# Optimization experiments

Hardware: AMD Instinct MI355X
Metric: run time of the kernel (lower is better)

## Reference

```python
import jax, jax.numpy as jnp
import numpy as np
from jax import lax

B, IN, H1, H2, NC = 16384, 128, 256, 128, 10
BETA = 0.5
THR = 1.0
SLOPE = 25.0  # snntorch surrogate.fast_sigmoid default slope


@jax.custom_vjp
def spike(x):
    # Heaviside fire with fast-sigmoid surrogate gradient
    return (x > 0).astype(x.dtype)

def _spike_fwd(x):
    return spike(x), x

def _spike_bwd(x, g):
    return (g / (SLOPE * jnp.abs(x) + 1.0) ** 2,)

spike.defvjp(_spike_fwd, _spike_bwd)


def setup_inputs() -> dict:
    key = jax.random.key(0)
    ks = jax.random.split(key, 7)
    def lin(kw, kb, fan_in, fan_out):
        lim = 1.0 / np.sqrt(fan_in)
        W = jax.random.uniform(kw, (fan_out, fan_in), jnp.float32, -lim, lim)
        b = jax.random.uniform(kb, (fan_out,), jnp.float32, -lim, lim)
        return W, b
    W1, b1 = lin(ks[0], ks[1], IN, H1)
    W2, b2 = lin(ks[2], ks[3], H1, H2)
    Wo, bo = lin(ks[4], ks[5], H2, NC)
    x = jax.random.normal(ks[6], (B, IN), jnp.float32)
    return {"x": x, "W1": W1, "b1": b1, "W2": W2, "b2": b2,
            "Wo": Wo, "bo": bo, "num_steps": 20}


def reference(x, W1, b1, W2, b2, Wo, bo, num_steps):
    # fc1(x) is time-invariant -> hoist out of the recurrent loop (same math)
    cur1 = x @ W1.T + b1  # [B, H1]

    def lif(mem, cur):
        # snntorch Leaky (reset_mechanism='subtract'):
        # reset from previous mem (detached), then decay+input, then fire
        reset = lax.stop_gradient((mem > THR).astype(mem.dtype))
        mem = BETA * mem + cur - reset * THR
        spk = spike(mem - THR)
        return spk, mem

    def step(carry, _):
        m1, m2, mo = carry
        s1, m1 = lif(m1, cur1)
        s2, m2 = lif(m2, s1 @ W2.T + b2)
        so, mo = lif(mo, s2 @ Wo.T + bo)
        return (m1, m2, mo), so

    init = (jnp.zeros((B, H1), x.dtype),
            jnp.zeros((B, H2), x.dtype),
            jnp.zeros((B, NC), x.dtype))
    _, spk_rec = lax.scan(step, init, None, length=num_steps)
    return spk_rec.sum(axis=0)  # [B, NC] spike counts
```

## Files before the change

### kernel.cpp

```cpp
#include <hip/hip_runtime.h>
#include <stdint.h>

#define B_TOT 16384
#define IN_DIM 128
#define H1 256
#define H2 128
#define NC 10

#define W2T_BYTES (H1 * H2 * 4)
#define WOT_OFF   W2T_BYTES
#define WOT_BYTES (H2 * NC * 4)
#define SCR_OFF   (WOT_OFF + WOT_BYTES)
#define LDS_BYTES (SCR_OFF + 16 * 1024)

typedef float v2f __attribute__((ext_vector_type(2)));

__global__ __launch_bounds__(256) void gemm1_kernel(
    const float* __restrict__ x, const float* __restrict__ W1,
    const float* __restrict__ b1, float* __restrict__ cur1) {
  __shared__ float xs[16 * 128];
  const int tid = threadIdx.x;
  const long row0 = (long)blockIdx.x * 16;

  const float4* xt = (const float4*)(x + row0 * IN_DIM);
  float4* xs4 = (float4*)xs;
  xs4[tid] = xt[tid];
  xs4[tid + 256] = xt[tid + 256];
  __syncthreads();

  const int n = tid;
  float acc[16];
#pragma unroll
  for (int r = 0; r < 16; ++r) acc[r] = 0.f;

  const float* wrow = W1 + n * IN_DIM;
  for (int k0 = 0; k0 < IN_DIM; k0 += 4) {
    const float4 wv = *(const float4*)(wrow + k0);
#pragma unroll
    for (int r = 0; r < 16; ++r) {
      const float4 xv = *(const float4*)(xs + r * IN_DIM + k0);
      acc[r] = fmaf(wv.x, xv.x, acc[r]);
      acc[r] = fmaf(wv.y, xv.y, acc[r]);
      acc[r] = fmaf(wv.z, xv.z, acc[r]);
      acc[r] = fmaf(wv.w, xv.w, acc[r]);
    }
  }
  const float bias = b1[n];
#pragma unroll
  for (int r = 0; r < 16; ++r)
    cur1[(row0 + r) * H1 + n] = acc[r] + bias;
}

__global__ __launch_bounds__(1024) void transpose_kernel(
    const float* __restrict__ W2, const float* __restrict__ Wo,
    float* __restrict__ W2T, float* __restrict__ WoT) {
  const int idx = blockIdx.x * 1024 + threadIdx.x;
  if (idx < H2 * H1) {
    const int o = idx >> 8;
    const int j = idx & 255;
    W2T[j * H2 + o] = W2[idx];
  } else {
    const int k = idx - H2 * H1;
    if (k < NC * H2) {
      const int o = k >> 7;
      const int j = k & 127;
      WoT[j * NC + o] = Wo[k];
    }
  }
}

__device__ __forceinline__ int mbcnt64(unsigned long long m) {
  return (int)__builtin_amdgcn_mbcnt_hi(
      (unsigned)(m >> 32), __builtin_amdgcn_mbcnt_lo((unsigned)m, 0u));
}

__global__ __launch_bounds__(1024) void snn_kernel(
    const float* __restrict__ cur1,
    const float* __restrict__ W2Tg, const float* __restrict__ WoTg,
    const float* __restrict__ W2, const float* __restrict__ Wo,
    const float* __restrict__ x, const float* __restrict__ W1,
    const float* __restrict__ b1,
    const float* __restrict__ b2, const float* __restrict__ bo,
    const int* __restrict__ nsp, float* __restrict__ out) {
  extern __shared__ float lds[];
  float* w2t = lds;
  float* wot = lds + H1 * H2;

  const int tid = threadIdx.x;
  if (W2Tg != nullptr) {
    float4* dst = (float4*)w2t;
    const float4* src = (const float4*)W2Tg;
#pragma unroll
    for (int i = 0; i < 8; ++i) dst[tid + i * 1024] = src[tid + i * 1024];
    if (tid < 320) ((float4*)wot)[tid] = ((const float4*)WoTg)[tid];
  } else {
    for (int idx = tid; idx < H2 * H1; idx += 1024) {
      const int o = idx >> 8;
      const int j = idx & 255;
      w2t[j * H2 + o] = W2[idx];
    }
    for (int idx = tid; idx < NC * H2; idx += 1024) {
      const int o = idx >> 7;
      const int j = idx & 127;
      wot[j * NC + o] = Wo[idx];
    }
  }
  __syncthreads();

  const int w = tid >> 6;
  const int l = tid & 63;
  const int lo = (l < NC) ? l : 0;
  const float bb0 = b2[2 * l];
  const float bb1 = b2[2 * l + 1];
  const float bol = bo[lo];
  const int nsteps = *nsp;

  int* scr = (int*)((char*)lds + SCR_OFF) + w * 256;
  const char* w2b = (const char*)lds + 8 * l;
  const char* wob = (const char*)lds + WOT_OFF + 4 * lo;

  const int wr0 = l << 9;
  const int wr1 = (64 + l) << 9;
  const int wr2 = (128 + l) << 9;
  const int wr3 = (192 + l) << 9;
  const int or0 = 80 * l;
  const int or1 = 80 * l + 40;

#define MAIN_B8()                                     \
  {                                                   \
    const int4 ia = *(const int4*)(scr + k);          \
    const int4 ib = *(const int4*)(scr + k + 4);      \
    const v2f p0 = *(const v2f*)(w2b + ia.x);         \
    const v2f p1 = *(const v2f*)(w2b + ia.y);         \
    const v2f p2 = *(const v2f*)(w2b + ia.z);         \
    const v2f p3 = *(const v2f*)(w2b + ia.w);         \
    const v2f p4 = *(const v2f*)(w2b + ib.x);         \
    const v2f p5 = *(const v2f*)(w2b + ib.y);         \
    const v2f p6 = *(const v2f*)(w2b + ib.z);         \
    const v2f p7 = *(const v2f*)(w2b + ib.w);         \
    acc += p0; acc += p1; acc += p2; acc += p3;       \
    acc += p4; acc += p5; acc += p6; acc += p7;       \
  }

#define OUT_B8()                                      \
  {                                                   \
    const int4 ia = *(const int4*)(scr + k);          \
    const int4 ib = *(const int4*)(scr + k + 4);      \
    const float q0 = *(const float*)(wob + ia.x);     \
    const float q1 = *(const float*)(wob + ia.y);     \
    const float q2 = *(const float*)(wob + ia.z);     \
    const float q3 = *(const float*)(wob + ia.w);     \
    const float q4 = *(const float*)(wob + ib.x);     \
    const float q5 = *(const float*)(wob + ib.y);     \
    const float q6 = *(const float*)(wob + ib.z);     \
    const float q7 = *(const float*)(wob + ib.w);     \
    co += q0; co += q1; co += q2; co += q3;           \
    co += q4; co += q5; co += q6; co += q7;           \
  }

  for (int r = 0; r < 4; ++r) {
    const long b = (long)blockIdx.x * 64 + w * 4 + r;

    float c[4];
    if (cur1 != nullptr) {
#pragma unroll
      for (int i = 0; i < 4; ++i) c[i] = cur1[b * H1 + i * 64 + l];
    } else {
      const float* xr = x + b * IN_DIM;
#pragma unroll
      for (int i = 0; i < 4; ++i) {
        const int n = i * 64 + l;
        const float* wr = W1 + n * IN_DIM;
        float a = 0.f;
        for (int kk = 0; kk < IN_DIM; kk += 4) {
          const float4 wv = *(const float4*)(wr + kk);
          const float4 xv = *(const float4*)(xr + kk);
          a = fmaf(wv.x, xv.x, a);
          a = fmaf(wv.y, xv.y, a);
          a = fmaf(wv.z, xv.z, a);
          a = fmaf(wv.w, xv.w, a);
        }
        c[i] = a + b1[n];
      }
    }

    float m1[4] = {0.f, 0.f, 0.f, 0.f};
    float sp1[4] = {0.f, 0.f, 0.f, 0.f};
    float m2a = 0.f, m2b = 0.f, sp2a = 0.f, sp2b = 0.f;
    float mo = 0.f, spo = 0.f, cnt = 0.f;

    for (int t = 0; t < nsteps; ++t) {
      float n0 = fmaf(0.5f, m1[0], c[0]) - sp1[0];
      float n1 = fmaf(0.5f, m1[1], c[1]) - sp1[1];
      float n2 = fmaf(0.5f, m1[2], c[2]) - sp1[2];
      float n3 = fmaf(0.5f, m1[3], c[3]) - sp1[3];
      const bool s0 = n0 > 1.0f;
      const bool s1 = n1 > 1.0f;
      const bool s2 = n2 > 1.0f;
      const bool s3 = n3 > 1.0f;
      m1[0] = n0; m1[1] = n1; m1[2] = n2; m1[3] = n3;
      sp1[0] = s0 ? 1.0f : 0.0f;
      sp1[1] = s1 ? 1.0f : 0.0f;
      sp1[2] = s2 ? 1.0f : 0.0f;
      sp1[3] = s3 ? 1.0f : 0.0f;
      const unsigned long long g0 = __ballot(s0);
      const unsigned long long g1 = __ballot(s1);
      const unsigned long long g2 = __ballot(s2);
      const unsigned long long g3 = __ballot(s3);
      const int pc0 = (int)__popcll(g0);
      const int pc1 = (int)__popcll(g1);
      const int pc2 = (int)__popcll(g2);
      const int pc3 = (int)__popcll(g3);
      const int S = pc0 + pc1 + pc2 + pc3;

      if (s0) scr[mbcnt64(g0)] = wr0;
      if (s1) scr[pc0 + mbcnt64(g1)] = wr1;
      if (s2) scr[pc0 + pc1 + mbcnt64(g2)] = wr2;
      if (s3) scr[pc0 + pc1 + pc2 + mbcnt64(g3)] = wr3;
      asm volatile("s_waitcnt lgkmcnt(0)" ::: "memory");

      v2f acc = {0.f, 0.f};
      int k = 0;
      for (; k + 8 <= S; k += 8) MAIN_B8();
      if (S & 4) {
        const int4 ia = *(const int4*)(scr + k);
        const v2f p0 = *(const v2f*)(w2b + ia.x);
        const v2f p1 = *(const v2f*)(w2b + ia.y);
        const v2f p2 = *(const v2f*)(w2b + ia.z);
        const v2f p3 = *(const v2f*)(w2b + ia.w);
        acc += p0; acc += p1; acc += p2; acc += p3;
        k += 4;
      }
      if (S & 2) {
        const int2 ia = *(const int2*)(scr + k);
        const v2f p0 = *(const v2f*)(w2b + ia.x);
        const v2f p1 = *(const v2f*)(w2b + ia.y);
        acc += p0; acc += p1;
        k += 2;
      }
      if (S & 1) {
        const int i0 = scr[k];
        const v2f p0 = *(const v2f*)(w2b + i0);
        acc += p0;
      }
      const float a0 = acc.x + bb0;
      const float a1 = acc.y + bb1;

      m2a = fmaf(0.5f, m2a, a0) - sp2a;
      m2b = fmaf(0.5f, m2b, a1) - sp2b;
      const bool sa = m2a > 1.0f;
      const bool sb = m2b > 1.0f;
      const unsigned long long mA = __ballot(sa);
      const unsigned long long mB = __ballot(sb);
      sp2a = sa ? 1.0f : 0.0f;
      sp2b = sb ? 1.0f : 0.0f;
      const int pcA = (int)__popcll(mA);
      const int So = pcA + (int)__popcll(mB);

      if (sa) scr[mbcnt64(mA)] = or0;
      if (sb) scr[pcA + mbcnt64(mB)] = or1;
      asm volatile("s_waitcnt lgkmcnt(0)" ::: "memory");

      float co = 0.f;
      k = 0;
      for (; k + 8 <= So; k += 8) OUT_B8();
      if (So & 4) {
        const int4 ia = *(const int4*)(scr + k);
        const float q0 = *(const float*)(wob + ia.x);
        const float q1 = *(const float*)(wob + ia.y);
        const float q2 = *(const float*)(wob + ia.z);
        const float q3 = *(const float*)(wob + ia.w);
        co += q0; co += q1; co += q2; co += q3;
        k += 4;
      }
      if (So & 2) {
        const int2 ia = *(const int2*)(scr + k);
        const float q0 = *(const float*)(wob + ia.x);
        const float q1 = *(const float*)(wob + ia.y);
        co += q0; co += q1;
        k += 2;
      }
      if (So & 1) {
        const int i0 = scr[k];
        co += *(const float*)(wob + i0);
      }
      co += bol;

      mo = fmaf(0.5f, mo, co) - spo;
      const bool so = mo > 1.0f;
      spo = so ? 1.0f : 0.0f;
      cnt += spo;
    }

    if (l < NC) out[b * NC + l] = cnt;
  }
#undef MAIN_B8
#undef OUT_B8
}

extern "C" void kernel_launch(void* const* d_in, const int* in_sizes, int n_in,
                              void* d_out, int out_size, void* d_ws,
                              size_t ws_size, hipStream_t stream) {
  const float* x  = (const float*)d_in[0];
  const float* W1 = (const float*)d_in[1];
  const float* b1 = (const float*)d_in[2];
  const float* W2 = (const float*)d_in[3];
  const float* b2 = (const float*)d_in[4];
  const float* Wo = (const float*)d_in[5];
  const float* bo = (const float*)d_in[6];
  const int* nsp  = (const int*)d_in[7];
  float* outp = (float*)d_out;

  const size_t cur1_bytes = (size_t)B_TOT * H1 * sizeof(float);
  const size_t w2t_bytes  = (size_t)H1 * H2 * sizeof(float);
  const size_t wot_bytes  = (size_t)H2 * NC * sizeof(float);

  float* cur1 = nullptr;
  float* W2Tg = nullptr;
  float* WoTg = nullptr;

  if (ws_size >= cur1_bytes) {
    cur1 = (float*)d_ws;
    gemm1_kernel<<<B_TOT / 16, 256, 0, stream>>>(x, W1, b1, cur1);
  }
  if (ws_size >= cur1_bytes + w2t_bytes + wot_bytes) {
    W2Tg = (float*)((char*)d_ws + cur1_bytes);
    WoTg = W2Tg + H1 * H2;
    transpose_kernel<<<(H2 * H1 + NC * H2 + 1023) / 1024, 1024, 0, stream>>>(
        W2, Wo, W2Tg, WoTg);
  }

  hipFuncSetAttribute((const void*)snn_kernel,
                      hipFuncAttributeMaxDynamicSharedMemorySize, LDS_BYTES);
  snn_kernel<<<256, 1024, LDS_BYTES, stream>>>(cur1, W2Tg, WoTg, W2, Wo, x,
                                               W1, b1, b2, bo, nsp, outp);
}
```

Baseline: 121.1 us.

## Split W2 between LDS and global memory, gathering half via scalar loads

Only the first 128 rows of the transposed W2 now live in LDS, which shrinks the LDS footprint. Spikes from hidden units 128-255 are compacted into a separate scratch list, and their rows are read from global/L2 memory using wave-uniform offsets obtained with readfirstlane. The first 16 of these are prefetched unconditionally, with a zero row padded at offset ZG. The change aims to cut LDS traffic and bank pressure and possibly allow two blocks per CU, at the cost of global-memory latency inside the recurrent loop. The fallback paths for a missing workspace are removed.

```diff
diff --git a/kernel.cpp b/kernel.cpp
--- a/kernel.cpp
+++ b/kernel.cpp
@@ -7,11 +7,13 @@
 #define H2 128
 #define NC 10
 
-#define W2T_BYTES (H1 * H2 * 4)
-#define WOT_OFF   W2T_BYTES
-#define WOT_BYTES (H2 * NC * 4)
-#define SCR_OFF   (WOT_OFF + WOT_BYTES)
-#define LDS_BYTES (SCR_OFF + 16 * 1024)
+#define W2TL_BYTES (128 * H2 * 4)
+#define WOT_OFF    W2TL_BYTES
+#define WOT_BYTES  (H2 * NC * 4)
+#define SCR_OFF    (WOT_OFF + WOT_BYTES)
+#define LDS_BYTES  (SCR_OFF + 16 * 1024)
+
+#define ZG 131072
 
 typedef float v2f __attribute__((ext_vector_type(2)));
 
@@ -59,13 +61,13 @@
     const int o = idx >> 8;
     const int j = idx & 255;
     W2T[j * H2 + o] = W2[idx];
-  } else {
-    const int k = idx - H2 * H1;
-    if (k < NC * H2) {
-      const int o = k >> 7;
-      const int j = k & 127;
-      WoT[j * NC + o] = Wo[k];
-    }
+  } else if (idx < H2 * H1 + H2) {
+    W2T[idx] = 0.f;
+  } else if (idx < H2 * H1 + H2 + NC * H2) {
+    const int k = idx - (H2 * H1 + H2);
+    const int o = k >> 7;
+    const int j = k & 127;
+    WoT[j * NC + o] = Wo[k];
   }
 }
 
@@ -75,35 +77,20 @@
 }
 
 __global__ __launch_bounds__(1024) void snn_kernel(
-    const float* __restrict__ cur1,
-    const float* __restrict__ W2Tg, const float* __restrict__ WoTg,
-    const float* __restrict__ W2, const float* __restrict__ Wo,
-    const float* __restrict__ x, const float* __restrict__ W1,
-    const float* __restrict__ b1,
-    const float* __restrict__ b2, const float* __restrict__ bo,
-    const int* __restrict__ nsp, float* __restrict__ out) {
+    const float* __restrict__ cur1, const float* __restrict__ W2Tg,
+    const float* __restrict__ WoTg, const float* __restrict__ b2,
+    const float* __restrict__ bo, const int* __restrict__ nsp,
+    float* __restrict__ out) {
   extern __shared__ float lds[];
-  float* w2t = lds;
-  float* wot = lds + H1 * H2;
 
   const int tid = threadIdx.x;
-  if (W2Tg != nullptr) {
-    float4* dst = (float4*)w2t;
+  {
+    float4* dst = (float4*)lds;
     const float4* src = (const float4*)W2Tg;
 #pragma unroll
-    for (int i = 0; i < 8; ++i) dst[tid + i * 1024] = src[tid + i * 1024];
-    if (tid < 320) ((float4*)wot)[tid] = ((const float4*)WoTg)[tid];
-  } else {
-    for (int idx = tid; idx < H2 * H1; idx += 1024) {
-      const int o = idx >> 8;
-      const int j = idx & 255;
-      w2t[j * H2 + o] = W2[idx];
-    }
-    for (int idx = tid; idx < NC * H2; idx += 1024) {
-      const int o = idx >> 7;
-      const int j = idx & 127;
-      wot[j * NC + o] = Wo[idx];
-    }
+    for (int i = 0; i < 4; ++i) dst[tid + i * 1024] = src[tid + i * 1024];
+    if (tid < 320)
+      ((float4*)((char*)lds + WOT_OFF))[tid] = ((const float4*)WoTg)[tid];
   }
   __syncthreads();
 
@@ -115,21 +102,23 @@
   const float bol = bo[lo];
   const int nsteps = *nsp;
 
-  int* scr = (int*)((char*)lds + SCR_OFF) + w * 256;
+  int* scrL = (int*)((char*)lds + SCR_OFF) + w * 256;
+  int* scrG = scrL + 128;
   const char* w2b = (const char*)lds + 8 * l;
+  const char* w2g = (const char*)W2Tg + 8 * l;
   const char* wob = (const char*)lds + WOT_OFF + 4 * lo;
 
   const int wr0 = l << 9;
   const int wr1 = (64 + l) << 9;
-  const int wr2 = (128 + l) << 9;
-  const int wr3 = (192 + l) << 9;
+  const int gr2 = (128 + l) << 9;
+  const int gr3 = (192 + l) << 9;
   const int or0 = 80 * l;
   const int or1 = 80 * l + 40;
 
-#define MAIN_B8()                                     \
+#define LDS_B8()                                      \
   {                                                   \
-    const int4 ia = *(const int4*)(scr + k);          \
-    const int4 ib = *(const int4*)(scr + k + 4);      \
+    const int4 ia = *(const int4*)(scrL + k);         \
+    const int4 ib = *(const int4*)(scrL + k + 4);     \
     const v2f p0 = *(const v2f*)(w2b + ia.x);         \
     const v2f p1 = *(const v2f*)(w2b + ia.y);         \
     const v2f p2 = *(const v2f*)(w2b + ia.z);         \
@@ -144,8 +133,8 @@
 
 #define OUT_B8()                                      \
   {                                                   \
-    const int4 ia = *(const int4*)(scr + k);          \
-    const int4 ib = *(const int4*)(scr + k + 4);      \
+    const int4 ia = *(const int4*)(scrL + k);         \
+    const int4 ib = *(const int4*)(scrL + k + 4);     \
     const float q0 = *(const float*)(wob + ia.x);     \
     const float q1 = *(const float*)(wob + ia.y);     \
     const float q2 = *(const float*)(wob + ia.z);     \
@@ -158,31 +147,16 @@
     co += q4; co += q5; co += q6; co += q7;           \
   }
 
+#define GSEL(reg, vec_comp, i)                                   \
+  int reg = __builtin_amdgcn_readfirstlane(vec_comp);            \
+  reg = (i < SG) ? reg : ZG;
+
   for (int r = 0; r < 4; ++r) {
     const long b = (long)blockIdx.x * 64 + w * 4 + r;
 
     float c[4];
-    if (cur1 != nullptr) {
-#pragma unroll
-      for (int i = 0; i < 4; ++i) c[i] = cur1[b * H1 + i * 64 + l];
-    } else {
-      const float* xr = x + b * IN_DIM;
-#pragma unroll
-      for (int i = 0; i < 4; ++i) {
-        const int n = i * 64 + l;
-        const float* wr = W1 + n * IN_DIM;
-        float a = 0.f;
-        for (int kk = 0; kk < IN_DIM; kk += 4) {
-          const float4 wv = *(const float4*)(wr + kk);
-          const float4 xv = *(const float4*)(xr + kk);
-          a = fmaf(wv.x, xv.x, a);
-          a = fmaf(wv.y, xv.y, a);
-          a = fmaf(wv.z, xv.z, a);
-          a = fmaf(wv.w, xv.w, a);
-        }
-        c[i] = a + b1[n];
-      }
-    }
+#pragma unroll
+    for (int i = 0; i < 4; ++i) c[i] = cur1[b * H1 + i * 64 + l];
 
     float m1[4] = {0.f, 0.f, 0.f, 0.f};
     float sp1[4] = {0.f, 0.f, 0.f, 0.f};
@@ -211,19 +185,45 @@
       const int pc1 = (int)__popcll(g1);
       const int pc2 = (int)__popcll(g2);
       const int pc3 = (int)__popcll(g3);
-      const int S = pc0 + pc1 + pc2 + pc3;
-
-      if (s0) scr[mbcnt64(g0)] = wr0;
-      if (s1) scr[pc0 + mbcnt64(g1)] = wr1;
-      if (s2) scr[pc0 + pc1 + mbcnt64(g2)] = wr2;
-      if (s3) scr[pc0 + pc1 + pc2 + mbcnt64(g3)] = wr3;
+      const int SL = pc0 + pc1;
+      const int SG = pc2 + pc3;
+
+      if (s0) scrL[mbcnt64(g0)] = wr0;
+      if (s1) scrL[pc0 + mbcnt64(g1)] = wr1;
+      if (s2) scrG[mbcnt64(g2)] = gr2;
+      if (s3) scrG[pc2 + mbcnt64(g3)] = gr3;
       asm volatile("s_waitcnt lgkmcnt(0)" ::: "memory");
+
+      const int4 ga = *(const int4*)(scrG);
+      const int4 gb = *(const int4*)(scrG + 4);
+      const int4 gc = *(const int4*)(scrG + 8);
+      const int4 gd = *(const int4*)(scrG + 12);
+      GSEL(o0, ga.x, 0)  GSEL(o1, ga.y, 1)  GSEL(o2, ga.z, 2)  GSEL(o3, ga.w, 3)
+      GSEL(o4, gb.x, 4)  GSEL(o5, gb.y, 5)  GSEL(o6, gb.z, 6)  GSEL(o7, gb.w, 7)
+      GSEL(o8, gc.x, 8)  GSEL(o9, gc.y, 9)  GSEL(o10, gc.z, 10) GSEL(o11, gc.w, 11)
+      GSEL(o12, gd.x, 12) GSEL(o13, gd.y, 13) GSEL(o14, gd.z, 14) GSEL(o15, gd.w, 15)
+      const v2f q0 = *(const v2f*)(w2g + o0);
+      const v2f q1 = *(const v2f*)(w2g + o1);
+      const v2f q2 = *(const v2f*)(w2g + o2);
+      const v2f q3 = *(const v2f*)(w2g + o3);
+      const v2f q4 = *(const v2f*)(w2g + o4);
+      const v2f q5 = *(const v2f*)(w2g + o5);
+      const v2f q6 = *(const v2f*)(w2g + o6);
+      const v2f q7 = *(const v2f*)(w2g + o7);
+      const v2f q8 = *(const v2f*)(w2g + o8);
+      const v2f q9 = *(const v2f*)(w2g + o9);
+      const v2f q10 = *(const v2f*)(w2g + o10);
+      const v2f q11 = *(const v2f*)(w2g + o11);
+      const v2f q12 = *(const v2f*)(w2g + o12);
+      const v2f q13 = *(const v2f*)(w2g + o13);
+      const v2f q14 = *(const v2f*)(w2g + o14);
+      const v2f q15 = *(const v2f*)(w2g + o15);
 
       v2f acc = {0.f, 0.f};
       int k = 0;
-      for (; k + 8 <= S; k += 8) MAIN_B8();
-      if (S & 4) {
-        const int4 ia = *(const int4*)(scr + k);
+      for (; k + 8 <= SL; k += 8) LDS_B8();
+      if (SL & 4) {
+        const int4 ia = *(const int4*)(scrL + k);
         const v2f p0 = *(const v2f*)(w2b + ia.x);
         const v2f p1 = *(const v2f*)(w2b + ia.y);
         const v2f p2 = *(const v2f*)(w2b + ia.z);
@@ -231,17 +231,26 @@
         acc += p0; acc += p1; acc += p2; acc += p3;
         k += 4;
       }
-      if (S & 2) {
-        const int2 ia = *(const int2*)(scr + k);
+      if (SL & 2) {
+        const int2 ia = *(const int2*)(scrL + k);
         const v2f p0 = *(const v2f*)(w2b + ia.x);
         const v2f p1 = *(const v2f*)(w2b + ia.y);
         acc += p0; acc += p1;
         k += 2;
       }
-      if (S & 1) {
-        const int i0 = scr[k];
-        const v2f p0 = *(const v2f*)(w2b + i0);
+      if (SL & 1) {
+        const v2f p0 = *(const v2f*)(w2b + scrL[k]);
         acc += p0;
+      }
+
+      acc += q0;  acc += q1;  acc += q2;  acc += q3;
+      acc += q4;  acc += q5;  acc += q6;  acc += q7;
+      acc += q8;  acc += q9;  acc += q10; acc += q11;
+      acc += q12; acc += q13; acc += q14; acc += q15;
+      for (int k2 = 16; k2 < SG; ++k2) {
+        const int o = __builtin_amdgcn_readfirstlane(scrG[k2]);
+        const v2f qq = *(const v2f*)(w2g + o);
+        acc += qq;
       }
       const float a0 = acc.x + bb0;
       const float a1 = acc.y + bb1;
@@ -257,32 +266,31 @@
       const int pcA = (int)__popcll(mA);
       const int So = pcA + (int)__popcll(mB);
 
-      if (sa) scr[mbcnt64(mA)] = or0;
-      if (sb) scr[pcA + mbcnt64(mB)] = or1;
+      if (sa) scrL[mbcnt64(mA)] = or0;
+      if (sb) scrL[pcA + mbcnt64(mB)] = or1;
       asm volatile("s_waitcnt lgkmcnt(0)" ::: "memory");
 
       float co = 0.f;
       k = 0;
       for (; k + 8 <= So; k += 8) OUT_B8();
       if (So & 4) {
-        const int4 ia = *(const int4*)(scr + k);
-        const float q0 = *(const float*)(wob + ia.x);
-        const float q1 = *(const float*)(wob + ia.y);
-        const float q2 = *(const float*)(wob + ia.z);
-        const float q3 = *(const float*)(wob + ia.w);
-        co += q0; co += q1; co += q2; co += q3;
+        const int4 ia = *(const int4*)(scrL + k);
+        const float u0 = *(const float*)(wob + ia.x);
+        const float u1 = *(const float*)(wob + ia.y);
+        const float u2 = *(const float*)(wob + ia.z);
+        const float u3 = *(const float*)(wob + ia.w);
+        co += u0; co += u1; co += u2; co += u3;
         k += 4;
       }
       if (So & 2) {
-        const int2 ia = *(const int2*)(scr + k);
-        const float q0 = *(const float*)(wob + ia.x);
-        const float q1 = *(const float*)(wob + ia.y);
-        co += q0; co += q1;
+        const int2 ia = *(const int2*)(scrL + k);
+        const float u0 = *(const float*)(wob + ia.x);
+        const float u1 = *(const float*)(wob + ia.y);
+        co += u0; co += u1;
         k += 2;
       }
       if (So & 1) {
-        const int i0 = scr[k];
-        co += *(const float*)(wob + i0);
+        co += *(const float*)(wob + scrL[k]);
       }
       co += bol;
 
@@ -294,8 +302,9 @@
 
     if (l < NC) out[b * NC + l] = cnt;
   }
-#undef MAIN_B8
+#undef LDS_B8
 #undef OUT_B8
+#undef GSEL
 }
 
 extern "C" void kernel_launch(void* const* d_in, const int* in_sizes, int n_in,
@@ -311,27 +320,16 @@
   const int* nsp  = (const int*)d_in[7];
   float* outp = (float*)d_out;
 
-  const size_t cur1_bytes = (size_t)B_TOT * H1 * sizeof(float);
-  const size_t w2t_bytes  = (size_t)H1 * H2 * sizeof(float);
-  const size_t wot_bytes  = (size_t)H2 * NC * sizeof(float);
-
-  float* cur1 = nullptr;
-  float* W2Tg = nullptr;
-  float* WoTg = nullptr;
-
-  if (ws_size >= cur1_bytes) {
-    cur1 = (float*)d_ws;
-    gemm1_kernel<<<B_TOT / 16, 256, 0, stream>>>(x, W1, b1, cur1);
-  }
-  if (ws_size >= cur1_bytes + w2t_bytes + wot_bytes) {
-    W2Tg = (float*)((char*)d_ws + cur1_bytes);
-    WoTg = W2Tg + H1 * H2;
-    transpose_kernel<<<(H2 * H1 + NC * H2 + 1023) / 1024, 1024, 0, stream>>>(
-        W2, Wo, W2Tg, WoTg);
-  }
+  float* cur1 = (float*)d_ws;
+  float* W2Tg = cur1 + (size_t)B_TOT * H1;
+  float* WoTg = W2Tg + H1 * H2 + H2;
+
+  gemm1_kernel<<<B_TOT / 16, 256, 0, stream>>>(x, W1, b1, cur1);
+  transpose_kernel<<<(H2 * H1 + H2 + NC * H2 + 1023) / 1024, 1024, 0,
+                     stream>>>(W2, Wo, W2Tg, WoTg);
 
   hipFuncSetAttribute((const void*)snn_kernel,
                       hipFuncAttributeMaxDynamicSharedMemorySize, LDS_BYTES);
-  snn_kernel<<<256, 1024, LDS_BYTES, stream>>>(cur1, W2Tg, WoTg, W2, Wo, x,
-                                               W1, b1, b2, bo, nsp, outp);
-}
+  snn_kernel<<<256, 1024, LDS_BYTES, stream>>>(cur1, W2Tg, WoTg, b2, bo, nsp,
+                                               outp);
+}
```

After: 210.1 us. 73.5% more time.
